# Optimization experiments

Hardware: AMD Instinct MI355X
Metric: run time of the kernel (lower is better)

The kernel has to match this reference:

```python
import jax, jax.numpy as jnp
import numpy as np

B, T = 16, 1024
ACTION_DIM, HIDDEN = 2048, 256
ADJ_STRENGTH = 0.1
SMOOTH = 0.9
CRIT_W = jnp.array([0.25, 0.75], dtype=jnp.float32)
NONCRIT_W = jnp.array([0.75, 0.25], dtype=jnp.float32)
LN_EPS = 1e-5


def _xavier_uniform(key, fan_in, fan_out, gain=0.1):
    limit = gain * np.sqrt(6.0 / (fan_in + fan_out))
    return jax.random.uniform(key, (fan_in, fan_out), minval=-limit, maxval=limit, dtype=jnp.float32)


def setup_inputs() -> dict:
    key = jax.random.key(0)
    ks = jax.random.split(key, 6)
    critical_labels = jax.random.randint(ks[0], (B, T), 0, 2)
    action_tokens = jax.random.normal(ks[1], (B, T, ACTION_DIM), dtype=jnp.float32)
    H2 = HIDDEN // 2
    return {
        'critical_labels': critical_labels,
        'action_tokens': action_tokens,
        'W1': _xavier_uniform(ks[2], ACTION_DIM, HIDDEN),
        'b1': jnp.zeros((HIDDEN,), jnp.float32),
        'g1': jnp.ones((HIDDEN,), jnp.float32),
        'be1': jnp.zeros((HIDDEN,), jnp.float32),
        'W2': _xavier_uniform(ks[3], HIDDEN, H2),
        'b2': jnp.zeros((H2,), jnp.float32),
        'g2': jnp.ones((H2,), jnp.float32),
        'be2': jnp.zeros((H2,), jnp.float32),
        'W3': _xavier_uniform(ks[4], H2, 2),
        'b3': jnp.zeros((2,), jnp.float32),
        'temperature': jnp.asarray(1.0, jnp.float32),
    }


def _layernorm(x, g, b):
    mu = jnp.mean(x, axis=-1, keepdims=True)
    var = jnp.var(x, axis=-1, keepdims=True)
    return (x - mu) * jax.lax.rsqrt(var + LN_EPS) * g + b


def reference(critical_labels, action_tokens, W1, b1, g1, be1, W2, b2, g2, be2, W3, b3, temperature):
    # base weights from binary labels: (B,T,2)
    crit = (critical_labels > 0)[..., None]
    base = jnp.where(crit, CRIT_W, NONCRIT_W)
    # MLP gate (dropout inactive in eval): Linear-LN-GELU x2, Linear, Tanh
    h = jax.nn.gelu(_layernorm(action_tokens @ W1 + b1, g1, be1), approximate=False)
    h = jax.nn.gelu(_layernorm(h @ W2 + b2, g2, be2), approximate=False)
    adjustments = jnp.tanh(h @ W3 + b3) * ADJ_STRENGTH
    temp = jnp.clip(temperature, 0.1, None)
    adjusted = jax.nn.softmax((base + adjustments) / temp, axis=-1)
    # temporal EMA smoothing: default state has prev_weights batch=1 != B, so t=0 passes through
    def step(s, c):
        s = SMOOTH * s + (1.0 - SMOOTH) * c
        return s, s
    init = adjusted[:, 0]                              # (B,2)
    _, rest = jax.lax.scan(step, init, jnp.swapaxes(adjusted[:, 1:], 0, 1))
    smoothed = jnp.concatenate([adjusted[:, :1], jnp.swapaxes(rest, 0, 1)], axis=1)
    return smoothed
```

## Files before the change

### kernel.cpp

```cpp
#include <hip/hip_runtime.h>
#include <hip/hip_bf16.h>
#include <math.h>

typedef __bf16 bf16x8 __attribute__((ext_vector_type(8)));
typedef float  f32x4  __attribute__((ext_vector_type(4)));

#define MFMA16(a,b,c) __builtin_amdgcn_mfma_f32_16x16x32_bf16(a,b,c,0,0,0)

__device__ __forceinline__ float gelu_exact(float x){
    return 0.5f * x * (1.0f + erff(x * 0.7071067811865476f));
}

__global__ void transp_bf16(const float* __restrict__ src, __bf16* __restrict__ dst,
                            int K, int N){
    int k0 = blockIdx.x * 8;
    int n  = threadIdx.x;
    if (n >= N) return;
    bf16x8 v;
#pragma unroll
    for (int r = 0; r < 8; ++r)
        v[r] = (__bf16)src[(size_t)(k0 + r) * N + n];
    *(bf16x8*)&dst[(size_t)n * K + k0] = v;
}

__global__ __launch_bounds__(256) void gemm1_ln_gelu(
    const float* __restrict__ X, const __bf16* __restrict__ W1T,
    const float* __restrict__ b1, const float* __restrict__ g1,
    const float* __restrict__ be1, __bf16* __restrict__ H1)
{
    __shared__ __bf16 lA[2][64*64];
    __shared__ __bf16 lB[2][256*64];
    __shared__ float  redS[64][4];
    __shared__ float  redQ[64][4];

    const int tid  = threadIdx.x;
    const int wid  = tid >> 6;
    const int lane = tid & 63;
    const int l15  = lane & 15;
    const int lg   = lane >> 4;
    const int mBase = blockIdx.x * 64;

    const int sRow = tid >> 3;
    const int sC8  = (tid & 7) * 8;
    const int sDst = sRow * 64 + (sC8 ^ ((sRow & 7) << 3));
    const float*  aSrc = X   + (size_t)(mBase + sRow) * 2048 + sC8;
    const __bf16* bSrc = W1T + (size_t)sRow * 2048 + sC8;

    f32x4 acc[4][4] = {};

#pragma unroll
    for (int i = 0; i < 2; ++i){
        const float4* p = (const float4*)(aSrc + (size_t)i*32*2048);
        float4 f0 = p[0], f1 = p[1];
        bf16x8 v;
        v[0]=(__bf16)f0.x; v[1]=(__bf16)f0.y; v[2]=(__bf16)f0.z; v[3]=(__bf16)f0.w;
        v[4]=(__bf16)f1.x; v[5]=(__bf16)f1.y; v[6]=(__bf16)f1.z; v[7]=(__bf16)f1.w;
        *(bf16x8*)&lA[0][sDst + i*32*64] = v;
    }
#pragma unroll
    for (int i = 0; i < 8; ++i){
        bf16x8 v = *(const bf16x8*)(bSrc + (size_t)i*32*2048);
        *(bf16x8*)&lB[0][sDst + i*32*64] = v;
    }
    __syncthreads();

    for (int s = 0; s < 32; ++s){
        const int cur  = s & 1;
        const bool more = (s < 31);
        const int kN = (s + 1) * 64;
        float4 fA[2][2];
        bf16x8 fB[8];
        if (more){
#pragma unroll
            for (int i = 0; i < 2; ++i){
                const float4* p = (const float4*)(aSrc + (size_t)i*32*2048 + kN);
                fA[i][0] = p[0]; fA[i][1] = p[1];
            }
#pragma unroll
            for (int i = 0; i < 8; ++i)
                fB[i] = *(const bf16x8*)(bSrc + (size_t)i*32*2048 + kN);
        }
#pragma unroll
        for (int kk = 0; kk < 2; ++kk){
            const int kcol = kk*32 + lg*8;
            bf16x8 av[4], bv[4];
#pragma unroll
            for (int m = 0; m < 4; ++m){
                int row = m*16 + l15;
                av[m] = *(const bf16x8*)&lA[cur][row*64 + (kcol ^ ((row&7)<<3))];
            }
#pragma unroll
            for (int n = 0; n < 4; ++n){
                int row = wid*64 + n*16 + l15;
                bv[n] = *(const bf16x8*)&lB[cur][row*64 + (kcol ^ ((row&7)<<3))];
            }
#pragma unroll
            for (int m = 0; m < 4; ++m)
#pragma unroll
                for (int n = 0; n < 4; ++n)
                    acc[m][n] = MFMA16(av[m], bv[n], acc[m][n]);
        }
        if (more){
            const int nxt = cur ^ 1;
#pragma unroll
            for (int i = 0; i < 2; ++i){
                bf16x8 v;
                v[0]=(__bf16)fA[i][0].x; v[1]=(__bf16)fA[i][0].y;
                v[2]=(__bf16)fA[i][0].z; v[3]=(__bf16)fA[i][0].w;
                v[4]=(__bf16)fA[i][1].x; v[5]=(__bf16)fA[i][1].y;
                v[6]=(__bf16)fA[i][1].z; v[7]=(__bf16)fA[i][1].w;
                *(bf16x8*)&lA[nxt][sDst + i*32*64] = v;
            }
#pragma unroll
            for (int i = 0; i < 8; ++i)
                *(bf16x8*)&lB[nxt][sDst + i*32*64] = fB[i];
        }
        __syncthreads();
    }

    float bias_[4], g1_[4], be_[4];
#pragma unroll
    for (int n = 0; n < 4; ++n){
        int col = wid*64 + n*16 + l15;
        bias_[n] = b1[col]; g1_[n] = g1[col]; be_[n] = be1[col];
    }
#pragma unroll
    for (int m = 0; m < 4; ++m)
#pragma unroll
        for (int n = 0; n < 4; ++n)
#pragma unroll
            for (int r = 0; r < 4; ++r)
                acc[m][n][r] += bias_[n];

#pragma unroll
    for (int m = 0; m < 4; ++m)
#pragma unroll
        for (int r = 0; r < 4; ++r){
            float s = 0.f, q = 0.f;
#pragma unroll
            for (int n = 0; n < 4; ++n){ float v = acc[m][n][r]; s += v; q += v*v; }
#pragma unroll
            for (int off = 1; off <= 8; off <<= 1){
                s += __shfl_xor(s, off, 64);
                q += __shfl_xor(q, off, 64);
            }
            int row = m*16 + lg*4 + r;
            if (l15 == 0){ redS[row][wid] = s; redQ[row][wid] = q; }
        }
    __syncthreads();

#pragma unroll
    for (int m = 0; m < 4; ++m)
#pragma unroll
        for (int r = 0; r < 4; ++r){
            int row = m*16 + lg*4 + r;
            float su = redS[row][0]+redS[row][1]+redS[row][2]+redS[row][3];
            float qu = redQ[row][0]+redQ[row][1]+redQ[row][2]+redQ[row][3];
            float mu  = su * (1.f/256.f);
            float var = qu * (1.f/256.f) - mu*mu;
            float rs  = rsqrtf(var + 1e-5f);
            size_t base = (size_t)(mBase + row) * 256;
#pragma unroll
            for (int n = 0; n < 4; ++n){
                float x  = acc[m][n][r];
                float xn = (x - mu) * rs * g1_[n] + be_[n];
                H1[base + wid*64 + n*16 + l15] = (__bf16)gelu_exact(xn);
            }
        }
}

__global__ __launch_bounds__(512) void tail_fused(
    const __bf16* __restrict__ H1, const __bf16* __restrict__ W2T,
    const float* __restrict__ b2, const float* __restrict__ g2,
    const float* __restrict__ be2, const float* __restrict__ W3,
    const float* __restrict__ b3, const int* __restrict__ labels,
    const float* __restrict__ temperature, float* __restrict__ ADJ)
{
    __shared__ union { __bf16 lH[64*256]; float h2[64*128]; } u;
    __shared__ __bf16 lW[128*256];
    __shared__ float  redS[64][4];
    __shared__ float  redQ[64][4];
    __shared__ float  lw3[256];

    const int tid  = threadIdx.x;
    const int wid  = tid >> 6;
    const int lane = tid & 63;
    const int l15  = lane & 15;
    const int lg   = lane >> 4;
    const int wm   = wid >> 2, wn = wid & 3;
    const int mBase = blockIdx.x * 64;

    {
        int r0 = tid >> 5;
        int c8 = (tid & 31) * 8;
        int swz = c8 ^ ((r0 & 7) << 3);
#pragma unroll
        for (int i = 0; i < 4; ++i){
            int row = r0 + i*16;
            bf16x8 v = *(const bf16x8*)&H1[(size_t)(mBase+row)*256 + c8];
            *(bf16x8*)&u.lH[row*256 + swz] = v;
        }
#pragma unroll
        for (int i = 0; i < 8; ++i){
            int row = r0 + i*16;
            bf16x8 v = *(const bf16x8*)&W2T[(size_t)row*256 + c8];
            *(bf16x8*)&lW[row*256 + swz] = v;
        }
        if (tid < 256) lw3[tid] = W3[tid];
    }
    __syncthreads();

    f32x4 acc[2][2] = {};
#pragma unroll
    for (int kk = 0; kk < 8; ++kk){
        const int kcol = kk*32 + lg*8;
        bf16x8 av[2], bv[2];
#pragma unroll
        for (int m = 0; m < 2; ++m){
            int row = wm*32 + m*16 + l15;
            av[m] = *(const bf16x8*)&u.lH[row*256 + (kcol ^ ((row&7)<<3))];
        }
#pragma unroll
        for (int n = 0; n < 2; ++n){
            int row = wn*32 + n*16 + l15;
            bv[n] = *(const bf16x8*)&lW[row*256 + (kcol ^ ((row&7)<<3))];
        }
#pragma unroll
        for (int m = 0; m < 2; ++m)
#pragma unroll
            for (int n = 0; n < 2; ++n)
                acc[m][n] = MFMA16(av[m], bv[n], acc[m][n]);
    }

    float b2_[2], g2_[2], be_[2];
#pragma unroll
    for (int n = 0; n < 2; ++n){
        int col = wn*32 + n*16 + l15;
        b2_[n] = b2[col]; g2_[n] = g2[col]; be_[n] = be2[col];
    }
#pragma unroll
    for (int m = 0; m < 2; ++m)
#pragma unroll
        for (int n = 0; n < 2; ++n)
#pragma unroll
            for (int r = 0; r < 4; ++r)
                acc[m][n][r] += b2_[n];

#pragma unroll
    for (int m = 0; m < 2; ++m)
#pragma unroll
        for (int r = 0; r < 4; ++r){
            float s = 0.f, q = 0.f;
#pragma unroll
            for (int n = 0; n < 2; ++n){ float v = acc[m][n][r]; s += v; q += v*v; }
#pragma unroll
            for (int off = 1; off <= 8; off <<= 1){
                s += __shfl_xor(s, off, 64);
                q += __shfl_xor(q, off, 64);
            }
            int row = wm*32 + m*16 + lg*4 + r;
            if (l15 == 0){ redS[row][wn] = s; redQ[row][wn] = q; }
        }
    __syncthreads();

#pragma unroll
    for (int m = 0; m < 2; ++m)
#pragma unroll
        for (int r = 0; r < 4; ++r){
            int row = wm*32 + m*16 + lg*4 + r;
            float su = redS[row][0]+redS[row][1]+redS[row][2]+redS[row][3];
            float qu = redQ[row][0]+redQ[row][1]+redQ[row][2]+redQ[row][3];
            float mu  = su * (1.f/128.f);
            float var = qu * (1.f/128.f) - mu*mu;
            float rs  = rsqrtf(var + 1e-5f);
#pragma unroll
            for (int n = 0; n < 2; ++n){
                int col = wn*32 + n*16 + l15;
                float x = acc[m][n][r];
                float h = gelu_exact((x - mu)*rs*g2_[n] + be_[n]);
                u.h2[row*128 + (col ^ (row & 31))] = h;
            }
        }
    __syncthreads();

    if (tid < 64){
        const int row = tid;
        const int g = mBase + row;
        float a0 = b3[0], a1 = b3[1];
        for (int k = 0; k < 128; ++k){
            float v = u.h2[row*128 + (k ^ (row & 31))];
            a0 += v * lw3[2*k];
            a1 += v * lw3[2*k+1];
        }
        float t = fmaxf(temperature[0], 0.1f);
        float adj0 = tanhf(a0) * 0.1f;
        float adj1 = tanhf(a1) * 0.1f;
        bool crit = labels[g] > 0;
        float base0 = crit ? 0.25f : 0.75f;
        float base1 = crit ? 0.75f : 0.25f;
        float L0 = (base0 + adj0) / t, L1 = (base1 + adj1) / t;
        float mm = fmaxf(L0, L1);
        float e0 = expf(L0 - mm), e1 = expf(L1 - mm);
        float inv = 1.f / (e0 + e1);
        ADJ[(size_t)g*2    ] = e0 * inv;
        ADJ[(size_t)g*2 + 1] = e1 * inv;
    }
}

__global__ void ema_kernel(const float* __restrict__ ADJ, float* __restrict__ out)
{
    __shared__ float wtab[128];
    __shared__ float abuf[384*2];
    const int b     = blockIdx.x >> 2;
    const int chunk = blockIdx.x & 3;
    const int c0    = chunk * 256;
    const int tid   = threadIdx.x;
    if (tid < 128) wtab[tid] = powf(0.9f, (float)tid);
    for (int idx = tid; idx < 768; idx += 256){
        int tt = c0 - 128 + (idx >> 1);
        int cc = idx & 1;
        abuf[idx] = (tt >= 0) ? ADJ[((size_t)b*1024 + tt)*2 + cc] : 0.f;
    }
    __syncthreads();
#pragma unroll
    for (int i = 0; i < 2; ++i){
        int item = tid + i*256;
        int tl = item >> 1, cc = item & 1;
        int t = c0 + tl;
        int kmax = min(t, 127);
        float sum = 0.f;
        for (int k = 0; k <= kmax; ++k){
            float coef = (t - k == 0) ? wtab[k] : 0.1f * wtab[k];
            sum += coef * abuf[(tl - k + 128)*2 + cc];
        }
        out[((size_t)b*1024 + t)*2 + cc] = sum;
    }
}

extern "C" void kernel_launch(void* const* d_in, const int* in_sizes, int n_in,
                              void* d_out, int out_size, void* d_ws, size_t ws_size,
                              hipStream_t stream)
{
    const int*   labels = (const int*)  d_in[0];
    const float* X      = (const float*)d_in[1];
    const float* W1     = (const float*)d_in[2];
    const float* b1     = (const float*)d_in[3];
    const float* g1     = (const float*)d_in[4];
    const float* be1    = (const float*)d_in[5];
    const float* W2     = (const float*)d_in[6];
    const float* b2     = (const float*)d_in[7];
    const float* g2     = (const float*)d_in[8];
    const float* be2    = (const float*)d_in[9];
    const float* W3     = (const float*)d_in[10];
    const float* b3     = (const float*)d_in[11];
    const float* temp   = (const float*)d_in[12];
    float* out = (float*)d_out;

    char* ws = (char*)d_ws;
    __bf16* W1T = (__bf16*)(ws);
    __bf16* W2T = (__bf16*)(ws + 1048576);
    __bf16* H1  = (__bf16*)(ws + 1114112);
    float*  ADJ = (float*)(ws + 9502720);

    transp_bf16<<<256, 256, 0, stream>>>(W1, W1T, 2048, 256);
    transp_bf16<<<32,  256, 0, stream>>>(W2, W2T, 256, 128);
    gemm1_ln_gelu<<<256, 256, 0, stream>>>(X, W1T, b1, g1, be1, H1);
    tail_fused<<<256, 512, 0, stream>>>(H1, W2T, b2, g2, be2, W3, b3, labels, temp, ADJ);
    ema_kernel<<<64, 256, 0, stream>>>(ADJ, out);
}
```

Baseline: 91.99 us.

## Load W1 fragments straight to registers and split GEMM1 over 8 waves

The first GEMM no longer stages the 256x64 W1 tile in shared memory. Each wave loads its B fragments directly from global/L2 into registers, double-buffered across k-steps. The block grows to 512 threads arranged as a 2x4 wave grid, each wave owning 32 rows by 64 columns, which halves accumulator registers per wave and cuts LDS use to just the A tile. The cost is that W1 is fetched redundantly by both M-waves and loads are less coalesced, with latency now hidden only by register prefetch.

```diff
diff --git a/kernel.cpp b/kernel.cpp
--- a/kernel.cpp
+++ b/kernel.cpp
@@ -23,13 +23,12 @@
     *(bf16x8*)&dst[(size_t)n * K + k0] = v;
 }
 
-__global__ __launch_bounds__(256) void gemm1_ln_gelu(
+__global__ __launch_bounds__(512) void gemm1_ln_gelu(
     const float* __restrict__ X, const __bf16* __restrict__ W1T,
     const float* __restrict__ b1, const float* __restrict__ g1,
     const float* __restrict__ be1, __bf16* __restrict__ H1)
 {
     __shared__ __bf16 lA[2][64*64];
-    __shared__ __bf16 lB[2][256*64];
     __shared__ float  redS[64][4];
     __shared__ float  redQ[64][4];
 
@@ -38,94 +37,102 @@
     const int lane = tid & 63;
     const int l15  = lane & 15;
     const int lg   = lane >> 4;
+    const int wm   = wid >> 2;
+    const int wn   = wid & 3;
     const int mBase = blockIdx.x * 64;
 
     const int sRow = tid >> 3;
     const int sC8  = (tid & 7) * 8;
     const int sDst = sRow * 64 + (sC8 ^ ((sRow & 7) << 3));
-    const float*  aSrc = X   + (size_t)(mBase + sRow) * 2048 + sC8;
-    const __bf16* bSrc = W1T + (size_t)sRow * 2048 + sC8;
-
-    f32x4 acc[4][4] = {};
-
-#pragma unroll
-    for (int i = 0; i < 2; ++i){
-        const float4* p = (const float4*)(aSrc + (size_t)i*32*2048);
-        float4 f0 = p[0], f1 = p[1];
-        bf16x8 v;
-        v[0]=(__bf16)f0.x; v[1]=(__bf16)f0.y; v[2]=(__bf16)f0.z; v[3]=(__bf16)f0.w;
-        v[4]=(__bf16)f1.x; v[5]=(__bf16)f1.y; v[6]=(__bf16)f1.z; v[7]=(__bf16)f1.w;
-        *(bf16x8*)&lA[0][sDst + i*32*64] = v;
-    }
-#pragma unroll
-    for (int i = 0; i < 8; ++i){
-        bf16x8 v = *(const bf16x8*)(bSrc + (size_t)i*32*2048);
-        *(bf16x8*)&lB[0][sDst + i*32*64] = v;
-    }
-    __syncthreads();
-
-    for (int s = 0; s < 32; ++s){
-        const int cur  = s & 1;
-        const bool more = (s < 31);
-        const int kN = (s + 1) * 64;
-        float4 fA[2][2];
-        bf16x8 fB[8];
-        if (more){
-#pragma unroll
-            for (int i = 0; i < 2; ++i){
-                const float4* p = (const float4*)(aSrc + (size_t)i*32*2048 + kN);
-                fA[i][0] = p[0]; fA[i][1] = p[1];
-            }
-#pragma unroll
-            for (int i = 0; i < 8; ++i)
-                fB[i] = *(const bf16x8*)(bSrc + (size_t)i*32*2048 + kN);
-        }
-#pragma unroll
-        for (int kk = 0; kk < 2; ++kk){
-            const int kcol = kk*32 + lg*8;
-            bf16x8 av[4], bv[4];
-#pragma unroll
-            for (int m = 0; m < 4; ++m){
-                int row = m*16 + l15;
-                av[m] = *(const bf16x8*)&lA[cur][row*64 + (kcol ^ ((row&7)<<3))];
-            }
-#pragma unroll
-            for (int n = 0; n < 4; ++n){
-                int row = wid*64 + n*16 + l15;
-                bv[n] = *(const bf16x8*)&lB[cur][row*64 + (kcol ^ ((row&7)<<3))];
-            }
-#pragma unroll
-            for (int m = 0; m < 4; ++m)
-#pragma unroll
-                for (int n = 0; n < 4; ++n)
-                    acc[m][n] = MFMA16(av[m], bv[n], acc[m][n]);
-        }
-        if (more){
-            const int nxt = cur ^ 1;
-#pragma unroll
-            for (int i = 0; i < 2; ++i){
-                bf16x8 v;
-                v[0]=(__bf16)fA[i][0].x; v[1]=(__bf16)fA[i][0].y;
-                v[2]=(__bf16)fA[i][0].z; v[3]=(__bf16)fA[i][0].w;
-                v[4]=(__bf16)fA[i][1].x; v[5]=(__bf16)fA[i][1].y;
-                v[6]=(__bf16)fA[i][1].z; v[7]=(__bf16)fA[i][1].w;
-                *(bf16x8*)&lA[nxt][sDst + i*32*64] = v;
-            }
-#pragma unroll
-            for (int i = 0; i < 8; ++i)
-                *(bf16x8*)&lB[nxt][sDst + i*32*64] = fB[i];
-        }
+    const float* aSrc = X + (size_t)(mBase + sRow) * 2048 + sC8;
+
+    const __bf16* bP0 = W1T + (size_t)(wn*64 +  0 + l15) * 2048 + lg*8;
+    const __bf16* bP1 = W1T + (size_t)(wn*64 + 16 + l15) * 2048 + lg*8;
+    const __bf16* bP2 = W1T + (size_t)(wn*64 + 32 + l15) * 2048 + lg*8;
+    const __bf16* bP3 = W1T + (size_t)(wn*64 + 48 + l15) * 2048 + lg*8;
+
+    f32x4 acc[2][4] = {};
+    bf16x8 fB0[8], fB1[8];
+
+#define LOADB(FB, S)                                                        \
+    {                                                                       \
+        FB[0] = *(const bf16x8*)(bP0 + (S)*64);                             \
+        FB[1] = *(const bf16x8*)(bP1 + (S)*64);                             \
+        FB[2] = *(const bf16x8*)(bP2 + (S)*64);                             \
+        FB[3] = *(const bf16x8*)(bP3 + (S)*64);                             \
+        FB[4] = *(const bf16x8*)(bP0 + (S)*64 + 32);                        \
+        FB[5] = *(const bf16x8*)(bP1 + (S)*64 + 32);                        \
+        FB[6] = *(const bf16x8*)(bP2 + (S)*64 + 32);                        \
+        FB[7] = *(const bf16x8*)(bP3 + (S)*64 + 32);                        \
+    }
+
+#define LOADA(A0, A1, S)                                                    \
+    {                                                                       \
+        A0 = *(const float4*)(aSrc + (S)*64);                               \
+        A1 = *(const float4*)(aSrc + (S)*64 + 4);                           \
+    }
+
+#define WRITEA(BUF, A0, A1)                                                 \
+    {                                                                       \
+        bf16x8 v;                                                           \
+        v[0]=(__bf16)A0.x; v[1]=(__bf16)A0.y; v[2]=(__bf16)A0.z;            \
+        v[3]=(__bf16)A0.w; v[4]=(__bf16)A1.x; v[5]=(__bf16)A1.y;            \
+        v[6]=(__bf16)A1.z; v[7]=(__bf16)A1.w;                               \
+        *(bf16x8*)&lA[BUF][sDst] = v;                                       \
+    }
+
+#define COMPUTE(BUF, FB)                                                    \
+    {                                                                       \
+        _Pragma("unroll")                                                   \
+        for (int kk = 0; kk < 2; ++kk){                                     \
+            const int kcol = kk*32 + lg*8;                                  \
+            const int swz  = kcol ^ ((l15 & 7) << 3);                       \
+            const int r0   = wm*32 + l15;                                   \
+            bf16x8 av0 = *(const bf16x8*)&lA[BUF][ r0      *64 + swz];      \
+            bf16x8 av1 = *(const bf16x8*)&lA[BUF][(r0+16)  *64 + swz];      \
+            _Pragma("unroll")                                               \
+            for (int n = 0; n < 4; ++n){                                    \
+                acc[0][n] = MFMA16(av0, FB[kk*4+n], acc[0][n]);             \
+                acc[1][n] = MFMA16(av1, FB[kk*4+n], acc[1][n]);             \
+            }                                                               \
+        }                                                                   \
+    }
+
+    {
+        float4 a0, a1;
+        LOADA(a0, a1, 0);
+        LOADB(fB0, 0);
+        WRITEA(0, a0, a1);
+    }
+    __syncthreads();
+
+    for (int it = 0; it < 16; ++it){
+        const int s = 2*it;
+        float4 a0, a1;
+        LOADA(a0, a1, s+1);
+        LOADB(fB1, s+1);
+        COMPUTE(0, fB0);
+        WRITEA(1, a0, a1);
         __syncthreads();
+        if (it < 15){
+            LOADA(a0, a1, s+2);
+            LOADB(fB0, s+2);
+        }
+        COMPUTE(1, fB1);
+        if (it < 15){
+            WRITEA(0, a0, a1);
+        }
+        __syncthreads();
     }
 
     float bias_[4], g1_[4], be_[4];
 #pragma unroll
     for (int n = 0; n < 4; ++n){
-        int col = wid*64 + n*16 + l15;
+        int col = wn*64 + n*16 + l15;
         bias_[n] = b1[col]; g1_[n] = g1[col]; be_[n] = be1[col];
     }
 #pragma unroll
-    for (int m = 0; m < 4; ++m)
+    for (int m = 0; m < 2; ++m)
 #pragma unroll
         for (int n = 0; n < 4; ++n)
 #pragma unroll
@@ -133,7 +140,7 @@
                 acc[m][n][r] += bias_[n];
 
 #pragma unroll
-    for (int m = 0; m < 4; ++m)
+    for (int m = 0; m < 2; ++m)
 #pragma unroll
         for (int r = 0; r < 4; ++r){
             float s = 0.f, q = 0.f;
@@ -144,16 +151,16 @@
                 s += __shfl_xor(s, off, 64);
                 q += __shfl_xor(q, off, 64);
             }
-            int row = m*16 + lg*4 + r;
-            if (l15 == 0){ redS[row][wid] = s; redQ[row][wid] = q; }
-        }
-    __syncthreads();
-
-#pragma unroll
-    for (int m = 0; m < 4; ++m)
+            int row = wm*32 + m*16 + lg*4 + r;
+            if (l15 == 0){ redS[row][wn] = s; redQ[row][wn] = q; }
+        }
+    __syncthreads();
+
+#pragma unroll
+    for (int m = 0; m < 2; ++m)
 #pragma unroll
         for (int r = 0; r < 4; ++r){
-            int row = m*16 + lg*4 + r;
+            int row = wm*32 + m*16 + lg*4 + r;
             float su = redS[row][0]+redS[row][1]+redS[row][2]+redS[row][3];
             float qu = redQ[row][0]+redQ[row][1]+redQ[row][2]+redQ[row][3];
             float mu  = su * (1.f/256.f);
@@ -164,9 +171,13 @@
             for (int n = 0; n < 4; ++n){
                 float x  = acc[m][n][r];
                 float xn = (x - mu) * rs * g1_[n] + be_[n];
-                H1[base + wid*64 + n*16 + l15] = (__bf16)gelu_exact(xn);
+                H1[base + wn*64 + n*16 + l15] = (__bf16)gelu_exact(xn);
             }
         }
+#undef LOADB
+#undef LOADA
+#undef WRITEA
+#undef COMPUTE
 }
 
 __global__ __launch_bounds__(512) void tail_fused(
@@ -364,7 +375,7 @@
 
     transp_bf16<<<256, 256, 0, stream>>>(W1, W1T, 2048, 256);
     transp_bf16<<<32,  256, 0, stream>>>(W2, W2T, 256, 128);
-    gemm1_ln_gelu<<<256, 256, 0, stream>>>(X, W1T, b1, g1, be1, H1);
+    gemm1_ln_gelu<<<256, 512, 0, stream>>>(X, W1T, b1, g1, be1, H1);
     tail_fused<<<256, 512, 0, stream>>>(H1, W2T, b2, g2, be2, W3, b3, labels, temp, ADJ);
     ema_kernel<<<64, 256, 0, stream>>>(ADJ, out);
 }
```

Measured after the change: 107.4 us. 16.8% more time.

## Enlarge GEMM1 block tile to 128 rows with 8 waves in a 2x4 grid

Applied to the files above, without the earlier changes.

The first GEMM+LayerNorm+GELU kernel now handles 128 rows per block with 512 threads arranged as a 2x4 wave grid, instead of 64 rows with 4 waves. Each staged W1T tile is reused across twice as many rows, which halves the total weight traffic from L2. Load, store and compute are factored into macros, and the LayerNorm reduction is indexed by the wave's row and column position. The cost is that only 128 blocks launch, fewer than the GPU's CU count, so X-load bandwidth and occupancy may drop.

```diff
diff --git a/kernel.cpp b/kernel.cpp
--- a/kernel.cpp
+++ b/kernel.cpp
@@ -23,105 +23,96 @@
     *(bf16x8*)&dst[(size_t)n * K + k0] = v;
 }
 
-__global__ __launch_bounds__(256) void gemm1_ln_gelu(
+__global__ __launch_bounds__(512, 1) void gemm1_ln_gelu(
     const float* __restrict__ X, const __bf16* __restrict__ W1T,
     const float* __restrict__ b1, const float* __restrict__ g1,
     const float* __restrict__ be1, __bf16* __restrict__ H1)
 {
-    __shared__ __bf16 lA[2][64*64];
+    __shared__ __bf16 lA[2][128*64];
     __shared__ __bf16 lB[2][256*64];
-    __shared__ float  redS[64][4];
-    __shared__ float  redQ[64][4];
+    __shared__ float  redS[128][4];
+    __shared__ float  redQ[128][4];
 
     const int tid  = threadIdx.x;
     const int wid  = tid >> 6;
     const int lane = tid & 63;
     const int l15  = lane & 15;
     const int lg   = lane >> 4;
-    const int mBase = blockIdx.x * 64;
+    const int wm   = wid >> 2;
+    const int wn   = wid & 3;
+    const int mBase = blockIdx.x * 128;
 
     const int sRow = tid >> 3;
     const int sC8  = (tid & 7) * 8;
-    const int sDst = sRow * 64 + (sC8 ^ ((sRow & 7) << 3));
+    const int sSwz = sC8 ^ ((sRow & 7) << 3);
     const float*  aSrc = X   + (size_t)(mBase + sRow) * 2048 + sC8;
     const __bf16* bSrc = W1T + (size_t)sRow * 2048 + sC8;
 
     f32x4 acc[4][4] = {};
-
-#pragma unroll
-    for (int i = 0; i < 2; ++i){
-        const float4* p = (const float4*)(aSrc + (size_t)i*32*2048);
-        float4 f0 = p[0], f1 = p[1];
-        bf16x8 v;
-        v[0]=(__bf16)f0.x; v[1]=(__bf16)f0.y; v[2]=(__bf16)f0.z; v[3]=(__bf16)f0.w;
-        v[4]=(__bf16)f1.x; v[5]=(__bf16)f1.y; v[6]=(__bf16)f1.z; v[7]=(__bf16)f1.w;
-        *(bf16x8*)&lA[0][sDst + i*32*64] = v;
-    }
-#pragma unroll
-    for (int i = 0; i < 8; ++i){
-        bf16x8 v = *(const bf16x8*)(bSrc + (size_t)i*32*2048);
-        *(bf16x8*)&lB[0][sDst + i*32*64] = v;
-    }
+    float4 ar[4];
+    bf16x8 br[4];
+
+#define LOADG(S) {                                                           \
+        ar[0] = *(const float4*)(aSrc + (size_t)(S)*64);                     \
+        ar[1] = *(const float4*)(aSrc + (size_t)(S)*64 + 4);                 \
+        ar[2] = *(const float4*)(aSrc + (size_t)64*2048 + (size_t)(S)*64);   \
+        ar[3] = *(const float4*)(aSrc + (size_t)64*2048 + (size_t)(S)*64+4); \
+        _Pragma("unroll")                                                    \
+        for (int i = 0; i < 4; ++i)                                          \
+            br[i] = *(const bf16x8*)(bSrc + (size_t)i*64*2048 + (size_t)(S)*64); }
+
+#define WRITEL(BUF) {                                                        \
+        bf16x8 v0, v1;                                                       \
+        v0[0]=(__bf16)ar[0].x; v0[1]=(__bf16)ar[0].y; v0[2]=(__bf16)ar[0].z; \
+        v0[3]=(__bf16)ar[0].w; v0[4]=(__bf16)ar[1].x; v0[5]=(__bf16)ar[1].y; \
+        v0[6]=(__bf16)ar[1].z; v0[7]=(__bf16)ar[1].w;                        \
+        v1[0]=(__bf16)ar[2].x; v1[1]=(__bf16)ar[2].y; v1[2]=(__bf16)ar[2].z; \
+        v1[3]=(__bf16)ar[2].w; v1[4]=(__bf16)ar[3].x; v1[5]=(__bf16)ar[3].y; \
+        v1[6]=(__bf16)ar[3].z; v1[7]=(__bf16)ar[3].w;                        \
+        *(bf16x8*)&lA[BUF][ sRow      *64 + sSwz] = v0;                      \
+        *(bf16x8*)&lA[BUF][(sRow + 64)*64 + sSwz] = v1;                      \
+        _Pragma("unroll")                                                    \
+        for (int i = 0; i < 4; ++i)                                          \
+            *(bf16x8*)&lB[BUF][(sRow + i*64)*64 + sSwz] = br[i]; }
+
+#define COMPUTE(BUF) {                                                       \
+        _Pragma("unroll")                                                    \
+        for (int kk = 0; kk < 2; ++kk){                                      \
+            const int base = kk*32 + lg*8;                                   \
+            bf16x8 av[4], bv[4];                                             \
+            _Pragma("unroll")                                                \
+            for (int m = 0; m < 4; ++m){                                     \
+                int row = wm*64 + m*16 + l15;                                \
+                av[m] = *(const bf16x8*)&lA[BUF][row*64 + (base ^ ((row&7)<<3))]; \
+            }                                                                \
+            _Pragma("unroll")                                                \
+            for (int n = 0; n < 4; ++n){                                     \
+                int row = wn*64 + n*16 + l15;                                \
+                bv[n] = *(const bf16x8*)&lB[BUF][row*64 + (base ^ ((row&7)<<3))]; \
+            }                                                                \
+            _Pragma("unroll")                                                \
+            for (int m = 0; m < 4; ++m)                                      \
+                _Pragma("unroll")                                            \
+                for (int n = 0; n < 4; ++n)                                  \
+                    acc[m][n] = MFMA16(av[m], bv[n], acc[m][n]);             \
+        } }
+
+    LOADG(0);
+    WRITEL(0);
     __syncthreads();
 
     for (int s = 0; s < 32; ++s){
-        const int cur  = s & 1;
-        const bool more = (s < 31);
-        const int kN = (s + 1) * 64;
-        float4 fA[2][2];
-        bf16x8 fB[8];
-        if (more){
-#pragma unroll
-            for (int i = 0; i < 2; ++i){
-                const float4* p = (const float4*)(aSrc + (size_t)i*32*2048 + kN);
-                fA[i][0] = p[0]; fA[i][1] = p[1];
-            }
-#pragma unroll
-            for (int i = 0; i < 8; ++i)
-                fB[i] = *(const bf16x8*)(bSrc + (size_t)i*32*2048 + kN);
-        }
-#pragma unroll
-        for (int kk = 0; kk < 2; ++kk){
-            const int kcol = kk*32 + lg*8;
-            bf16x8 av[4], bv[4];
-#pragma unroll
-            for (int m = 0; m < 4; ++m){
-                int row = m*16 + l15;
-                av[m] = *(const bf16x8*)&lA[cur][row*64 + (kcol ^ ((row&7)<<3))];
-            }
-#pragma unroll
-            for (int n = 0; n < 4; ++n){
-                int row = wid*64 + n*16 + l15;
-                bv[n] = *(const bf16x8*)&lB[cur][row*64 + (kcol ^ ((row&7)<<3))];
-            }
-#pragma unroll
-            for (int m = 0; m < 4; ++m)
-#pragma unroll
-                for (int n = 0; n < 4; ++n)
-                    acc[m][n] = MFMA16(av[m], bv[n], acc[m][n]);
-        }
-        if (more){
-            const int nxt = cur ^ 1;
-#pragma unroll
-            for (int i = 0; i < 2; ++i){
-                bf16x8 v;
-                v[0]=(__bf16)fA[i][0].x; v[1]=(__bf16)fA[i][0].y;
-                v[2]=(__bf16)fA[i][0].z; v[3]=(__bf16)fA[i][0].w;
-                v[4]=(__bf16)fA[i][1].x; v[5]=(__bf16)fA[i][1].y;
-                v[6]=(__bf16)fA[i][1].z; v[7]=(__bf16)fA[i][1].w;
-                *(bf16x8*)&lA[nxt][sDst + i*32*64] = v;
-            }
-#pragma unroll
-            for (int i = 0; i < 8; ++i)
-                *(bf16x8*)&lB[nxt][sDst + i*32*64] = fB[i];
-        }
+        const int cur = s & 1;
+        if (s < 31) LOADG(s+1);
+        COMPUTE(cur);
+        if (s < 31) WRITEL(cur ^ 1);
         __syncthreads();
     }
 
     float bias_[4], g1_[4], be_[4];
 #pragma unroll
     for (int n = 0; n < 4; ++n){
-        int col = wid*64 + n*16 + l15;
+        int col = wn*64 + n*16 + l15;
         bias_[n] = b1[col]; g1_[n] = g1[col]; be_[n] = be1[col];
     }
 #pragma unroll
@@ -144,8 +135,8 @@
                 s += __shfl_xor(s, off, 64);
                 q += __shfl_xor(q, off, 64);
             }
-            int row = m*16 + lg*4 + r;
-            if (l15 == 0){ redS[row][wid] = s; redQ[row][wid] = q; }
+            int row = wm*64 + m*16 + lg*4 + r;
+            if (l15 == 0){ redS[row][wn] = s; redQ[row][wn] = q; }
         }
     __syncthreads();
 
@@ -153,7 +144,7 @@
     for (int m = 0; m < 4; ++m)
 #pragma unroll
         for (int r = 0; r < 4; ++r){
-            int row = m*16 + lg*4 + r;
+            int row = wm*64 + m*16 + lg*4 + r;
             float su = redS[row][0]+redS[row][1]+redS[row][2]+redS[row][3];
             float qu = redQ[row][0]+redQ[row][1]+redQ[row][2]+redQ[row][3];
             float mu  = su * (1.f/256.f);
@@ -164,9 +155,12 @@
             for (int n = 0; n < 4; ++n){
                 float x  = acc[m][n][r];
                 float xn = (x - mu) * rs * g1_[n] + be_[n];
-                H1[base + wid*64 + n*16 + l15] = (__bf16)gelu_exact(xn);
+                H1[base + wn*64 + n*16 + l15] = (__bf16)gelu_exact(xn);
             }
         }
+#undef LOADG
+#undef WRITEL
+#undef COMPUTE
 }
 
 __global__ __launch_bounds__(512) void tail_fused(
@@ -364,7 +358,7 @@
 
     transp_bf16<<<256, 256, 0, stream>>>(W1, W1T, 2048, 256);
     transp_bf16<<<32,  256, 0, stream>>>(W2, W2T, 256, 128);
-    gemm1_ln_gelu<<<256, 256, 0, stream>>>(X, W1T, b1, g1, be1, H1);
+    gemm1_ln_gelu<<<128, 512, 0, stream>>>(X, W1T, b1, g1, be1, H1);
     tail_fused<<<256, 512, 0, stream>>>(H1, W2T, b2, g2, be2, W3, b3, labels, temp, ADJ);
     ema_kernel<<<64, 256, 0, stream>>>(ADJ, out);
 }
```

Measured after the change: 100.6 us. +9.4%, slower.
